# Optimization experiments

Hardware: AMD Instinct MI355X
Metric: run time of the kernel (lower is better)

The kernel has to match this reference:

```python
import jax, jax.numpy as jnp
import numpy as np

# normalization module stand-ins (simple monotone scalings, as in the repo they
# are fixed elementwise rescalings of the raw quantities)
def norm_local_x(n):
    return n

def norm_unit_contraction(c):
    return c

def norm_local_N(N):
    return jnp.log1p(N.astype(jnp.float32))

norm_TNG_radii = norm_local_x
norm_local_v = norm_local_x
norm_local_v0 = norm_local_x

EPS = 1e-5


def setup_inputs() -> dict:
    key = jax.random.key(0)
    ks = jax.random.split(key, 12)
    B, T, ND, KB = 2, 1024, 256, 3
    K_IN, H, L = 19, 128, 128
    x0 = 0.3 * jax.random.normal(ks[0], (B, T, 3), dtype=jnp.float32)
    # DM positions in local frame, |x| must stay < 1.05 (assert in original)
    x = jax.random.uniform(ks[1], (B, T, ND, 3), dtype=jnp.float32) - 0.5
    N = jax.random.randint(ks[2], (B, T), 1, 512, dtype=jnp.int32)
    basis = jax.random.normal(ks[3], (B, KB, 3), dtype=jnp.float32)
    v = jax.random.normal(ks[4], (B, T, ND, 3), dtype=jnp.float32)
    P200c = 0.5 + jax.random.uniform(ks[5], (B,), dtype=jnp.float32)
    s = 0.1
    W0 = s * jax.random.normal(ks[6], (K_IN, H - 1), dtype=jnp.float32)
    b0 = jnp.zeros((H - 1,), jnp.float32)
    W1 = s * jax.random.normal(ks[7], (H, H), dtype=jnp.float32)
    b1 = jnp.zeros((H,), jnp.float32)
    W2 = s * jax.random.normal(ks[8], (H, L), dtype=jnp.float32)
    b2 = jnp.zeros((L,), jnp.float32)
    return {"x0": x0, "x": x, "N": N, "basis": basis, "v": v, "P200c": P200c,
            "W0": W0, "b0": b0, "W1": W1, "b1": b1, "W2": W2, "b2": b2}


def create_scalars(x0, x, N, basis, v):
    B, T, ND, _ = x.shape
    # velocities relative to local mean (halo -> local frame)
    v0 = jnp.mean(v, axis=2)                      # [B,T,3]
    vc = v - v0[:, :, None, :]                    # [B,T,ND,3]

    x_norm = jnp.linalg.norm(x, axis=-1, keepdims=True) + EPS     # [B,T,ND,1]
    xu = x / x_norm
    x0_norm = jnp.linalg.norm(x0, axis=-1, keepdims=True) + EPS   # [B,T,1]
    x0u = x0 / x0_norm
    v0_norm = jnp.linalg.norm(v0, axis=-1, keepdims=True) + EPS   # [B,T,1]
    v0u = v0 / v0_norm
    v_norm = jnp.linalg.norm(vc, axis=-1, keepdims=True) + EPS    # [B,T,ND,1]
    vu = vc / v_norm

    bc = lambda a: jnp.broadcast_to(a[:, :, None, :], (B, T, ND, a.shape[-1]))

    feats = [
        norm_local_x(x_norm),                                          # |x| [1]
        norm_unit_contraction(jnp.einsum('btnd,bkd->btnk', xu, basis)),# x.basis [3]
        jnp.broadcast_to(norm_local_N(N)[:, :, None, None], (B, T, ND, 1)),  # N [1]
        bc(norm_TNG_radii(x0_norm)),                                   # |x0| [1]
        bc(norm_unit_contraction(jnp.einsum('btd,bkd->btk', x0u, basis))),  # x0.basis [3]
        bc(norm_local_v0(v0_norm)),                                    # |v0| [1]
        bc(norm_unit_contraction(jnp.einsum('btd,bkd->btk', v0u, basis))),  # v0.basis [3]
        bc(norm_unit_contraction(jnp.sum(x0u * v0u, axis=-1, keepdims=True))),  # x0.v0 [1]
        norm_local_v(v_norm),                                          # |v| [1]
        norm_unit_contraction(jnp.einsum('btnd,bkd->btnk', vu, basis)),# v.basis [3]
        norm_unit_contraction(jnp.sum(xu * vu, axis=-1, keepdims=True)),  # x.v [1]
    ]
    return jnp.concatenate(feats, axis=-1)  # [B,T,ND,19]


def reference(x0, x, N, basis, v, P200c, W0, b0, W1, b1, W2, b2):
    scalars = create_scalars(x0, x, N, basis, v)          # [B,T,ND,19]
    h = jax.nn.leaky_relu(scalars @ W0 + b0)              # [B,T,ND,H-1]
    h = jnp.mean(h, axis=2)                               # pool -> [B,T,H-1]
    h = jnp.concatenate([h, norm_local_N(N)[..., None]], axis=-1)  # [B,T,H]
    h = jax.nn.leaky_relu(h @ W1 + b1)                    # [B,T,H]
    out = h @ W2 + b2                                     # [B,T,Nlatent]
    return (1.0 / P200c)[:, None, None] * out
```

## Files before the change

kernel.cpp:

```cpp
#include <hip/hip_runtime.h>
#include <hip/hip_bf16.h>
#include <math.h>

#define EPSV 1e-5f
#define HD   128
#define AROW 40
#define WROW 40

typedef __attribute__((ext_vector_type(8))) short bf16x8;
typedef __attribute__((ext_vector_type(4))) float f32x4;

__global__ __launch_bounds__(256, 2) void net_fused(
    const float* __restrict__ x0g, const float* __restrict__ xg,
    const int*   __restrict__ Ng,  const float* __restrict__ basisg,
    const float* __restrict__ vg,  const float* __restrict__ Pg,
    const float* __restrict__ W0,  const float* __restrict__ b0,
    const float* __restrict__ W1,  const float* __restrict__ b1,
    const float* __restrict__ W2,  const float* __restrict__ b2,
    float* __restrict__ out, int Tn, int NDn)
{
    __shared__ __align__(16) __hip_bfloat16 SA[256 * AROW];
    __shared__ __align__(16) __hip_bfloat16 Wt1[128 * WROW];
    __shared__ __align__(16) __hip_bfloat16 Wt2[128 * WROW];
    __shared__ float cvec[HD];
    __shared__ float part[4][HD];
    __shared__ float hvec[HD];
    __shared__ float h1vec[HD];
    __shared__ float tailred[2][HD];
    __shared__ float vred[4][3];

    const int bt   = blockIdx.x;
    const int b    = bt / Tn;
    const int tid  = threadIdx.x;
    const int lane = tid & 63;
    const int wave = tid >> 6;

    const long pbase = ((long)bt * NDn + tid) * 3;
    const float xi0 = xg[pbase+0], xi1 = xg[pbase+1], xi2 = xg[pbase+2];
    const float vi0 = vg[pbase+0], vi1 = vg[pbase+1], vi2 = vg[pbase+2];

    float s0 = vi0, s1 = vi1, s2 = vi2;
    #pragma unroll
    for (int off = 32; off > 0; off >>= 1) {
        s0 += __shfl_down(s0, off);
        s1 += __shfl_down(s1, off);
        s2 += __shfl_down(s2, off);
    }
    if (lane == 0) { vred[wave][0] = s0; vred[wave][1] = s1; vred[wave][2] = s2; }

    {
        const int RV[9] = {0, 1, 2, 3, 14, 15, 16, 17, 18};
        if (tid < 128) {
            const int n = tid;
            __hip_bfloat16* w1 = &Wt1[n * WROW];
            __hip_bfloat16* w2 = &Wt2[n * WROW];
            const __hip_bfloat16 z16 = __float2bfloat16(0.0f);
            #pragma unroll
            for (int kk = 0; kk < 9; ++kk) {
                const float wv = (n < 127) ? W0[RV[kk] * 127 + n] : 0.0f;
                const __hip_bfloat16 hi = __float2bfloat16(wv);
                const __hip_bfloat16 lo = __float2bfloat16(wv - __bfloat162float(hi));
                w1[kk] = hi;  w1[16 + kk] = hi;
                w2[kk] = lo;  w2[16 + kk] = lo;
            }
            #pragma unroll
            for (int kk = 9; kk < 16; ++kk) {
                w1[kk] = z16;  w1[kk + 16] = z16;
                w2[kk] = z16;  w2[kk + 16] = z16;
            }
        }
    }
    __syncthreads();

    const float inv_nd = 1.0f / (float)NDn;
    const float v00 = (vred[0][0]+vred[1][0]+vred[2][0]+vred[3][0]) * inv_nd;
    const float v01 = (vred[0][1]+vred[1][1]+vred[2][1]+vred[3][1]) * inv_nd;
    const float v02 = (vred[0][2]+vred[1][2]+vred[2][2]+vred[3][2]) * inv_nd;

    const float p0 = x0g[bt*3+0], p1 = x0g[bt*3+1], p2 = x0g[bt*3+2];
    float bas[3][3];
    #pragma unroll
    for (int k = 0; k < 3; ++k)
        #pragma unroll
        for (int c = 0; c < 3; ++c)
            bas[k][c] = basisg[(b*3 + k)*3 + c];

    const float x0n  = sqrtf(p0*p0 + p1*p1 + p2*p2) + EPSV;
    const float ix0n = 1.0f / x0n;
    const float x0u0 = p0*ix0n, x0u1 = p1*ix0n, x0u2 = p2*ix0n;

    const float v0n  = sqrtf(v00*v00 + v01*v01 + v02*v02) + EPSV;
    const float iv0n = 1.0f / v0n;
    const float v0u0 = v00*iv0n, v0u1 = v01*iv0n, v0u2 = v02*iv0n;

    const float logN = log1pf((float)Ng[bt]);

    if (tid < 128) {
        float c = 0.0f;
        if (tid < 127) {
            float fc[10];
            fc[0] = logN;
            fc[1] = x0n;
            fc[2] = x0u0*bas[0][0] + x0u1*bas[0][1] + x0u2*bas[0][2];
            fc[3] = x0u0*bas[1][0] + x0u1*bas[1][1] + x0u2*bas[1][2];
            fc[4] = x0u0*bas[2][0] + x0u1*bas[2][1] + x0u2*bas[2][2];
            fc[5] = v0n;
            fc[6] = v0u0*bas[0][0] + v0u1*bas[0][1] + v0u2*bas[0][2];
            fc[7] = v0u0*bas[1][0] + v0u1*bas[1][1] + v0u2*bas[1][2];
            fc[8] = v0u0*bas[2][0] + v0u1*bas[2][1] + v0u2*bas[2][2];
            fc[9] = x0u0*v0u0 + x0u1*v0u1 + x0u2*v0u2;
            c = b0[tid];
            #pragma unroll
            for (int i = 0; i < 10; ++i)
                c = fmaf(fc[i], W0[(4 + i) * 127 + tid], c);
        }
        cvec[tid] = c;
    }

    {
        const float xn  = sqrtf(xi0*xi0 + xi1*xi1 + xi2*xi2) + EPSV;
        const float ixn = 1.0f / xn;
        const float xu0 = xi0*ixn, xu1 = xi1*ixn, xu2 = xi2*ixn;

        const float c0 = vi0 - v00, c1 = vi1 - v01, c2 = vi2 - v02;
        const float vn  = sqrtf(c0*c0 + c1*c1 + c2*c2) + EPSV;
        const float ivn = 1.0f / vn;
        const float vu0 = c0*ivn, vu1 = c1*ivn, vu2 = c2*ivn;

        float f[9];
        f[0] = xn;
        f[1] = xu0*bas[0][0] + xu1*bas[0][1] + xu2*bas[0][2];
        f[2] = xu0*bas[1][0] + xu1*bas[1][1] + xu2*bas[1][2];
        f[3] = xu0*bas[2][0] + xu1*bas[2][1] + xu2*bas[2][2];
        f[4] = vn;
        f[5] = vu0*bas[0][0] + vu1*bas[0][1] + vu2*bas[0][2];
        f[6] = vu0*bas[1][0] + vu1*bas[1][1] + vu2*bas[1][2];
        f[7] = vu0*bas[2][0] + vu1*bas[2][1] + vu2*bas[2][2];
        f[8] = xu0*vu0 + xu1*vu1 + xu2*vu2;

        __hip_bfloat16* Ar = &SA[tid * AROW];
        const __hip_bfloat16 z16 = __float2bfloat16(0.0f);
        #pragma unroll
        for (int kk = 0; kk < 9; ++kk) {
            const __hip_bfloat16 hi = __float2bfloat16(f[kk]);
            Ar[kk]      = hi;
            Ar[16 + kk] = __float2bfloat16(f[kk] - __bfloat162float(hi));
        }
        #pragma unroll
        for (int kk = 9; kk < 16; ++kk) {
            Ar[kk]      = z16;
            Ar[kk + 16] = z16;
        }
    }
    __syncthreads();

    {
        const int quad = lane >> 4;
        const int lm   = lane & 15;

        bf16x8 bf1[8], bf2[8];
        float  cl[8];
        #pragma unroll
        for (int nt = 0; nt < 8; ++nt) {
            bf1[nt] = *reinterpret_cast<const bf16x8*>(&Wt1[(nt*16 + lm) * WROW + quad*8]);
            bf2[nt] = *reinterpret_cast<const bf16x8*>(&Wt2[(nt*16 + lm) * WROW + quad*8]);
            cl[nt]  = cvec[nt*16 + lm];
        }

        float pooled[8];
        #pragma unroll
        for (int nt = 0; nt < 8; ++nt) pooled[nt] = 0.0f;

        const f32x4 zero = {0.f, 0.f, 0.f, 0.f};
        #pragma unroll
        for (int mt = 0; mt < 4; ++mt) {
            const int particle = wave*64 + mt*16 + lm;
            const bf16x8 af = *reinterpret_cast<const bf16x8*>(&SA[particle * AROW + quad*8]);
            #pragma unroll
            for (int nt = 0; nt < 8; ++nt) {
                f32x4 acc = __builtin_amdgcn_mfma_f32_16x16x32_bf16(af, bf1[nt], zero, 0, 0, 0);
                acc = __builtin_amdgcn_mfma_f32_16x16x32_bf16(af, bf2[nt], acc, 0, 0, 0);
                float t = 0.0f;
                #pragma unroll
                for (int r = 0; r < 4; ++r) {
                    const float d = acc[r] + cl[nt];
                    t += fmaxf(d, 0.01f*d);
                }
                pooled[nt] += t;
            }
        }
        #pragma unroll
        for (int nt = 0; nt < 8; ++nt) {
            pooled[nt] += __shfl_xor(pooled[nt], 16);
            pooled[nt] += __shfl_xor(pooled[nt], 32);
        }
        if (lane < 16) {
            #pragma unroll
            for (int nt = 0; nt < 8; ++nt)
                part[wave][nt*16 + lane] = pooled[nt];
        }
    }
    __syncthreads();

    if (tid < HD) {
        const float p = part[0][tid] + part[1][tid] + part[2][tid] + part[3][tid];
        hvec[tid] = (tid < 127) ? p * inv_nd : logN;
    }
    __syncthreads();

    {
        const int j    = tid & 127;
        const int half = tid >> 7;
        const int kb   = half * 64;
        float a = 0.0f;
        #pragma unroll 8
        for (int k = 0; k < 64; ++k) a = fmaf(hvec[kb + k], W1[(kb + k)*HD + j], a);
        tailred[half][j] = a;
    }
    __syncthreads();
    if (tid < HD) {
        const float a = b1[tid] + tailred[0][tid] + tailred[1][tid];
        h1vec[tid] = fmaxf(a, 0.01f*a);
    }
    __syncthreads();

    {
        const int j    = tid & 127;
        const int half = tid >> 7;
        const int kb   = half * 64;
        float a = 0.0f;
        #pragma unroll 8
        for (int k = 0; k < 64; ++k) a = fmaf(h1vec[kb + k], W2[(kb + k)*HD + j], a);
        tailred[half][j] = a;
    }
    __syncthreads();
    if (tid < HD) {
        const float a = b2[tid] + tailred[0][tid] + tailred[1][tid];
        out[(long)bt * HD + tid] = a / Pg[b];
    }
}

extern "C" void kernel_launch(void* const* d_in, const int* in_sizes, int n_in,
                              void* d_out, int out_size, void* d_ws, size_t ws_size,
                              hipStream_t stream) {
    const float* x0    = (const float*)d_in[0];
    const float* x     = (const float*)d_in[1];
    const int*   N     = (const int*)  d_in[2];
    const float* basis = (const float*)d_in[3];
    const float* v     = (const float*)d_in[4];
    const float* P200c = (const float*)d_in[5];
    const float* W0    = (const float*)d_in[6];
    const float* b0    = (const float*)d_in[7];
    const float* W1    = (const float*)d_in[8];
    const float* b1    = (const float*)d_in[9];
    const float* W2    = (const float*)d_in[10];
    const float* b2    = (const float*)d_in[11];
    float* out = (float*)d_out;

    const int B  = in_sizes[5];
    const int T  = in_sizes[2] / B;
    const int ND = in_sizes[1] / (in_sizes[2] * 3);

    dim3 grid(B * T), block(256);
    hipLaunchKernelGGL(net_fused, grid, block, 0, stream,
                       x0, x, N, basis, v, P200c, W0, b0, W1, b1, W2, b2,
                       out, T, ND);
}
```

Baseline: 119.0 us.

## Precompute split-bf16 W0 and transposed W1/W2 in a prep kernel

Adds a small prep kernel that converts W0 into hi/lo bf16 MFMA operands and transposes W1/W2 into workspace once per call. The main kernel no longer builds these weight tiles in LDS, which frees shared memory, and it raises the occupancy hint to 4 blocks per CU. The MFMA loop is reordered to keep A fragments in registers and stream B fragments from global. The tail matvecs switch to one thread per output doing float4 dot products over transposed rows, which drops a reduction and a barrier. The cost is an extra launch, plus reading weights from global/L2 instead of LDS, with half the threads idle in the tail.

```diff
diff --git a/kernel.cpp b/kernel.cpp
--- a/kernel.cpp
+++ b/kernel.cpp
@@ -5,28 +5,57 @@
 #define EPSV 1e-5f
 #define HD   128
 #define AROW 40
-#define WROW 40
 
 typedef __attribute__((ext_vector_type(8))) short bf16x8;
 typedef __attribute__((ext_vector_type(4))) float f32x4;
 
-__global__ __launch_bounds__(256, 2) void net_fused(
+__global__ __launch_bounds__(256) void prep_weights(
+    const float* __restrict__ W0, const float* __restrict__ W1,
+    const float* __restrict__ W2, __hip_bfloat16* __restrict__ wt1,
+    __hip_bfloat16* __restrict__ wt2, float* __restrict__ w1t,
+    float* __restrict__ w2t)
+{
+    if (blockIdx.x == 0) {
+        const int RV[9] = {0, 1, 2, 3, 14, 15, 16, 17, 18};
+        for (int i = threadIdx.x; i < 128 * 32; i += 256) {
+            const int n  = i >> 5;
+            const int kk = i & 15;
+            float val = 0.0f;
+            if (n < 127 && kk < 9) val = W0[RV[kk] * 127 + n];
+            const __hip_bfloat16 hi = __float2bfloat16(val);
+            const __hip_bfloat16 lo = __float2bfloat16(val - __bfloat162float(hi));
+            wt1[i] = hi;
+            wt2[i] = lo;
+        }
+    } else {
+        const int base = (blockIdx.x - 1) * 2048;
+        for (int t = threadIdx.x; t < 2048; t += 256) {
+            const int idx = base + t;
+            const float* src = (idx < 16384) ? W1 : W2;
+            float*       dst = (idx < 16384) ? w1t : w2t;
+            const int e = idx & 16383;
+            const int j = e >> 7, k = e & 127;
+            dst[j * 128 + k] = src[k * 128 + j];
+        }
+    }
+}
+
+__global__ __launch_bounds__(256, 4) void net_fused(
     const float* __restrict__ x0g, const float* __restrict__ xg,
     const int*   __restrict__ Ng,  const float* __restrict__ basisg,
     const float* __restrict__ vg,  const float* __restrict__ Pg,
     const float* __restrict__ W0,  const float* __restrict__ b0,
-    const float* __restrict__ W1,  const float* __restrict__ b1,
-    const float* __restrict__ W2,  const float* __restrict__ b2,
+    const float* __restrict__ b1,  const float* __restrict__ b2,
+    const __hip_bfloat16* __restrict__ wt1g,
+    const __hip_bfloat16* __restrict__ wt2g,
+    const float* __restrict__ w1t, const float* __restrict__ w2t,
     float* __restrict__ out, int Tn, int NDn)
 {
     __shared__ __align__(16) __hip_bfloat16 SA[256 * AROW];
-    __shared__ __align__(16) __hip_bfloat16 Wt1[128 * WROW];
-    __shared__ __align__(16) __hip_bfloat16 Wt2[128 * WROW];
     __shared__ float cvec[HD];
     __shared__ float part[4][HD];
-    __shared__ float hvec[HD];
-    __shared__ float h1vec[HD];
-    __shared__ float tailred[2][HD];
+    __shared__ __align__(16) float hvec[HD];
+    __shared__ __align__(16) float h1vec[HD];
     __shared__ float vred[4][3];
 
     const int bt   = blockIdx.x;
@@ -47,29 +76,6 @@
         s2 += __shfl_down(s2, off);
     }
     if (lane == 0) { vred[wave][0] = s0; vred[wave][1] = s1; vred[wave][2] = s2; }
-
-    {
-        const int RV[9] = {0, 1, 2, 3, 14, 15, 16, 17, 18};
-        if (tid < 128) {
-            const int n = tid;
-            __hip_bfloat16* w1 = &Wt1[n * WROW];
-            __hip_bfloat16* w2 = &Wt2[n * WROW];
-            const __hip_bfloat16 z16 = __float2bfloat16(0.0f);
-            #pragma unroll
-            for (int kk = 0; kk < 9; ++kk) {
-                const float wv = (n < 127) ? W0[RV[kk] * 127 + n] : 0.0f;
-                const __hip_bfloat16 hi = __float2bfloat16(wv);
-                const __hip_bfloat16 lo = __float2bfloat16(wv - __bfloat162float(hi));
-                w1[kk] = hi;  w1[16 + kk] = hi;
-                w2[kk] = lo;  w2[16 + kk] = lo;
-            }
-            #pragma unroll
-            for (int kk = 9; kk < 16; ++kk) {
-                w1[kk] = z16;  w1[kk + 16] = z16;
-                w2[kk] = z16;  w2[kk + 16] = z16;
-            }
-        }
-    }
     __syncthreads();
 
     const float inv_nd = 1.0f / (float)NDn;
@@ -138,19 +144,21 @@
         f[7] = vu0*bas[2][0] + vu1*bas[2][1] + vu2*bas[2][2];
         f[8] = xu0*vu0 + xu1*vu1 + xu2*vu2;
 
-        __hip_bfloat16* Ar = &SA[tid * AROW];
-        const __hip_bfloat16 z16 = __float2bfloat16(0.0f);
+        __hip_bfloat16 row[32];
+        #pragma unroll
+        for (int kk = 0; kk < 32; ++kk) row[kk] = __float2bfloat16(0.0f);
         #pragma unroll
         for (int kk = 0; kk < 9; ++kk) {
             const __hip_bfloat16 hi = __float2bfloat16(f[kk]);
-            Ar[kk]      = hi;
-            Ar[16 + kk] = __float2bfloat16(f[kk] - __bfloat162float(hi));
-        }
-        #pragma unroll
-        for (int kk = 9; kk < 16; ++kk) {
-            Ar[kk]      = z16;
-            Ar[kk + 16] = z16;
-        }
+            row[kk]      = hi;
+            row[16 + kk] = __float2bfloat16(f[kk] - __bfloat162float(hi));
+        }
+        bf16x8* dst = reinterpret_cast<bf16x8*>(&SA[tid * AROW]);
+        const bf16x8* src = reinterpret_cast<const bf16x8*>(row);
+        dst[0] = src[0];
+        dst[1] = src[1];
+        dst[2] = src[2];
+        dst[3] = src[3];
     }
     __syncthreads();
 
@@ -158,46 +166,33 @@
         const int quad = lane >> 4;
         const int lm   = lane & 15;
 
-        bf16x8 bf1[8], bf2[8];
-        float  cl[8];
+        bf16x8 afr[4];
+        #pragma unroll
+        for (int mt = 0; mt < 4; ++mt)
+            afr[mt] = *reinterpret_cast<const bf16x8*>(
+                &SA[(wave*64 + mt*16 + lm) * AROW + quad*8]);
+
+        const f32x4 zero = {0.f, 0.f, 0.f, 0.f};
         #pragma unroll
         for (int nt = 0; nt < 8; ++nt) {
-            bf1[nt] = *reinterpret_cast<const bf16x8*>(&Wt1[(nt*16 + lm) * WROW + quad*8]);
-            bf2[nt] = *reinterpret_cast<const bf16x8*>(&Wt2[(nt*16 + lm) * WROW + quad*8]);
-            cl[nt]  = cvec[nt*16 + lm];
-        }
-
-        float pooled[8];
-        #pragma unroll
-        for (int nt = 0; nt < 8; ++nt) pooled[nt] = 0.0f;
-
-        const f32x4 zero = {0.f, 0.f, 0.f, 0.f};
-        #pragma unroll
-        for (int mt = 0; mt < 4; ++mt) {
-            const int particle = wave*64 + mt*16 + lm;
-            const bf16x8 af = *reinterpret_cast<const bf16x8*>(&SA[particle * AROW + quad*8]);
+            const int woff = ((nt*16 + lm) * 32 + quad*8);
+            const bf16x8 bh = *reinterpret_cast<const bf16x8*>(&wt1g[woff]);
+            const bf16x8 bl = *reinterpret_cast<const bf16x8*>(&wt2g[woff]);
+            const float  cl = cvec[nt*16 + lm];
+            float p = 0.0f;
             #pragma unroll
-            for (int nt = 0; nt < 8; ++nt) {
-                f32x4 acc = __builtin_amdgcn_mfma_f32_16x16x32_bf16(af, bf1[nt], zero, 0, 0, 0);
-                acc = __builtin_amdgcn_mfma_f32_16x16x32_bf16(af, bf2[nt], acc, 0, 0, 0);
-                float t = 0.0f;
+            for (int mt = 0; mt < 4; ++mt) {
+                f32x4 acc = __builtin_amdgcn_mfma_f32_16x16x32_bf16(afr[mt], bh, zero, 0, 0, 0);
+                acc = __builtin_amdgcn_mfma_f32_16x16x32_bf16(afr[mt], bl, acc, 0, 0, 0);
                 #pragma unroll
                 for (int r = 0; r < 4; ++r) {
-                    const float d = acc[r] + cl[nt];
-                    t += fmaxf(d, 0.01f*d);
+                    const float d = acc[r] + cl;
+                    p += fmaxf(d, 0.01f*d);
                 }
-                pooled[nt] += t;
             }
-        }
-        #pragma unroll
-        for (int nt = 0; nt < 8; ++nt) {
-            pooled[nt] += __shfl_xor(pooled[nt], 16);
-            pooled[nt] += __shfl_xor(pooled[nt], 32);
-        }
-        if (lane < 16) {
-            #pragma unroll
-            for (int nt = 0; nt < 8; ++nt)
-                part[wave][nt*16 + lane] = pooled[nt];
+            p += __shfl_xor(p, 16);
+            p += __shfl_xor(p, 32);
+            if (lane < 16) part[wave][nt*16 + lane] = p;
         }
     }
     __syncthreads();
@@ -208,34 +203,36 @@
     }
     __syncthreads();
 
-    {
-        const int j    = tid & 127;
-        const int half = tid >> 7;
-        const int kb   = half * 64;
-        float a = 0.0f;
+    if (tid < HD) {
+        float a = b1[tid];
+        const float4* wr = reinterpret_cast<const float4*>(&w1t[tid * 128]);
+        const float4* hv = reinterpret_cast<const float4*>(hvec);
         #pragma unroll 8
-        for (int k = 0; k < 64; ++k) a = fmaf(hvec[kb + k], W1[(kb + k)*HD + j], a);
-        tailred[half][j] = a;
-    }
-    __syncthreads();
+        for (int kk = 0; kk < 32; ++kk) {
+            const float4 h4 = hv[kk];
+            const float4 w4 = wr[kk];
+            a = fmaf(h4.x, w4.x, a);
+            a = fmaf(h4.y, w4.y, a);
+            a = fmaf(h4.z, w4.z, a);
+            a = fmaf(h4.w, w4.w, a);
+        }
+        h1vec[tid] = fmaxf(a, 0.01f*a);
+    }
+    __syncthreads();
+
     if (tid < HD) {
-        const float a = b1[tid] + tailred[0][tid] + tailred[1][tid];
-        h1vec[tid] = fmaxf(a, 0.01f*a);
-    }
-    __syncthreads();
-
-    {
-        const int j    = tid & 127;
-        const int half = tid >> 7;
-        const int kb   = half * 64;
-        float a = 0.0f;
+        float a = b2[tid];
+        const float4* wr = reinterpret_cast<const float4*>(&w2t[tid * 128]);
+        const float4* hv = reinterpret_cast<const float4*>(h1vec);
         #pragma unroll 8
-        for (int k = 0; k < 64; ++k) a = fmaf(h1vec[kb + k], W2[(kb + k)*HD + j], a);
-        tailred[half][j] = a;
-    }
-    __syncthreads();
-    if (tid < HD) {
-        const float a = b2[tid] + tailred[0][tid] + tailred[1][tid];
+        for (int kk = 0; kk < 32; ++kk) {
+            const float4 h4 = hv[kk];
+            const float4 w4 = wr[kk];
+            a = fmaf(h4.x, w4.x, a);
+            a = fmaf(h4.y, w4.y, a);
+            a = fmaf(h4.z, w4.z, a);
+            a = fmaf(h4.w, w4.w, a);
+        }
         out[(long)bt * HD + tid] = a / Pg[b];
     }
 }
@@ -261,8 +258,16 @@
     const int T  = in_sizes[2] / B;
     const int ND = in_sizes[1] / (in_sizes[2] * 3);
 
-    dim3 grid(B * T), block(256);
-    hipLaunchKernelGGL(net_fused, grid, block, 0, stream,
-                       x0, x, N, basis, v, P200c, W0, b0, W1, b1, W2, b2,
-                       out, T, ND);
+    char* ws = (char*)d_ws;
+    __hip_bfloat16* wt1 = (__hip_bfloat16*)(ws);
+    __hip_bfloat16* wt2 = (__hip_bfloat16*)(ws + 8192);
+    float*          w1t = (float*)(ws + 16384);
+    float*          w2t = (float*)(ws + 81920);
+
+    hipLaunchKernelGGL(prep_weights, dim3(17), dim3(256), 0, stream,
+                       W0, W1, W2, wt1, wt2, w1t, w2t);
+
+    hipLaunchKernelGGL(net_fused, dim3(B * T), dim3(256), 0, stream,
+                       x0, x, N, basis, v, P200c, W0, b0, b1, b2,
+                       wt1, wt2, w1t, w2t, out, T, ND);
 }
```

New measurement: 136.5 us. 1.15x slower.

## Split fused kernel into weight prep, per-halo pooling, and batched tail MLP

Applied to the files above, without the earlier changes.

Replaces the single per-halo kernel with three launches. A one-block kernel precomputes the split-bf16 W0 tiles once into workspace. A one-wave-per-halo kernel does the feature build and MFMA pooling over all 256 particles. A separate tail kernel runs the two dense layers over 16 halos per block so W1/W2 loads are shared across rows. This removes the per-block weight conversion and the barrier-heavy, single-row tail matvecs, at the cost of extra launches, a global round trip for pooled features, and less parallelism per halo. ND is now hard-coded to 256.

```diff
diff --git a/kernel.cpp b/kernel.cpp
--- a/kernel.cpp
+++ b/kernel.cpp
@@ -3,79 +3,78 @@
 #include <math.h>
 
 #define EPSV 1e-5f
-#define HD   128
 #define AROW 40
-#define WROW 40
+#define HSTR 129
 
 typedef __attribute__((ext_vector_type(8))) short bf16x8;
 typedef __attribute__((ext_vector_type(4))) float f32x4;
 
-__global__ __launch_bounds__(256, 2) void net_fused(
+__global__ __launch_bounds__(256) void prep_weights(
+    const float* __restrict__ W0,
+    __hip_bfloat16* __restrict__ wt1, __hip_bfloat16* __restrict__ wt2)
+{
+    const int RV[9] = {0, 1, 2, 3, 14, 15, 16, 17, 18};
+    for (int i = threadIdx.x; i < 128 * 32; i += 256) {
+        const int n  = i >> 5;
+        const int kk = i & 15;
+        float val = 0.0f;
+        if (n < 127 && kk < 9) val = W0[RV[kk] * 127 + n];
+        const __hip_bfloat16 hi = __float2bfloat16(val);
+        const __hip_bfloat16 lo = __float2bfloat16(val - __bfloat162float(hi));
+        wt1[i] = hi;
+        wt2[i] = lo;
+    }
+}
+
+__global__ __launch_bounds__(64, 2) void halo_pool(
     const float* __restrict__ x0g, const float* __restrict__ xg,
     const int*   __restrict__ Ng,  const float* __restrict__ basisg,
-    const float* __restrict__ vg,  const float* __restrict__ Pg,
-    const float* __restrict__ W0,  const float* __restrict__ b0,
-    const float* __restrict__ W1,  const float* __restrict__ b1,
-    const float* __restrict__ W2,  const float* __restrict__ b2,
-    float* __restrict__ out, int Tn, int NDn)
+    const float* __restrict__ vg,  const float* __restrict__ W0,
+    const float* __restrict__ b0,
+    const __hip_bfloat16* __restrict__ wt1g,
+    const __hip_bfloat16* __restrict__ wt2g,
+    float* __restrict__ hbuf, int Tn)
 {
     __shared__ __align__(16) __hip_bfloat16 SA[256 * AROW];
-    __shared__ __align__(16) __hip_bfloat16 Wt1[128 * WROW];
-    __shared__ __align__(16) __hip_bfloat16 Wt2[128 * WROW];
-    __shared__ float cvec[HD];
-    __shared__ float part[4][HD];
-    __shared__ float hvec[HD];
-    __shared__ float h1vec[HD];
-    __shared__ float tailred[2][HD];
-    __shared__ float vred[4][3];
+    __shared__ float cvec[128];
 
     const int bt   = blockIdx.x;
     const int b    = bt / Tn;
-    const int tid  = threadIdx.x;
-    const int lane = tid & 63;
-    const int wave = tid >> 6;
-
-    const long pbase = ((long)bt * NDn + tid) * 3;
-    const float xi0 = xg[pbase+0], xi1 = xg[pbase+1], xi2 = xg[pbase+2];
-    const float vi0 = vg[pbase+0], vi1 = vg[pbase+1], vi2 = vg[pbase+2];
-
-    float s0 = vi0, s1 = vi1, s2 = vi2;
-    #pragma unroll
-    for (int off = 32; off > 0; off >>= 1) {
-        s0 += __shfl_down(s0, off);
-        s1 += __shfl_down(s1, off);
-        s2 += __shfl_down(s2, off);
-    }
-    if (lane == 0) { vred[wave][0] = s0; vred[wave][1] = s1; vred[wave][2] = s2; }
-
-    {
-        const int RV[9] = {0, 1, 2, 3, 14, 15, 16, 17, 18};
-        if (tid < 128) {
-            const int n = tid;
-            __hip_bfloat16* w1 = &Wt1[n * WROW];
-            __hip_bfloat16* w2 = &Wt2[n * WROW];
-            const __hip_bfloat16 z16 = __float2bfloat16(0.0f);
-            #pragma unroll
-            for (int kk = 0; kk < 9; ++kk) {
-                const float wv = (n < 127) ? W0[RV[kk] * 127 + n] : 0.0f;
-                const __hip_bfloat16 hi = __float2bfloat16(wv);
-                const __hip_bfloat16 lo = __float2bfloat16(wv - __bfloat162float(hi));
-                w1[kk] = hi;  w1[16 + kk] = hi;
-                w2[kk] = lo;  w2[16 + kk] = lo;
-            }
-            #pragma unroll
-            for (int kk = 9; kk < 16; ++kk) {
-                w1[kk] = z16;  w1[kk + 16] = z16;
-                w2[kk] = z16;  w2[kk + 16] = z16;
-            }
-        }
-    }
-    __syncthreads();
-
-    const float inv_nd = 1.0f / (float)NDn;
-    const float v00 = (vred[0][0]+vred[1][0]+vred[2][0]+vred[3][0]) * inv_nd;
-    const float v01 = (vred[0][1]+vred[1][1]+vred[2][1]+vred[3][1]) * inv_nd;
-    const float v02 = (vred[0][2]+vred[1][2]+vred[2][2]+vred[3][2]) * inv_nd;
+    const int lane = threadIdx.x;
+    const int quad = lane >> 4;
+    const int lm   = lane & 15;
+
+    bf16x8 bh[8], bl[8];
+    #pragma unroll
+    for (int nt = 0; nt < 8; ++nt) {
+        const int woff = (nt*16 + lm) * 32 + quad * 8;
+        bh[nt] = *reinterpret_cast<const bf16x8*>(&wt1g[woff]);
+        bl[nt] = *reinterpret_cast<const bf16x8*>(&wt2g[woff]);
+    }
+
+    const long gbase = (long)bt * 256 * 3;
+    float px[4][3], pv[4][3];
+    #pragma unroll
+    for (int j = 0; j < 4; ++j) {
+        const int p = j*64 + lane;
+        #pragma unroll
+        for (int c = 0; c < 3; ++c) {
+            px[j][c] = xg[gbase + p*3 + c];
+            pv[j][c] = vg[gbase + p*3 + c];
+        }
+    }
+
+    float s0 = pv[0][0]+pv[1][0]+pv[2][0]+pv[3][0];
+    float s1 = pv[0][1]+pv[1][1]+pv[2][1]+pv[3][1];
+    float s2 = pv[0][2]+pv[1][2]+pv[2][2]+pv[3][2];
+    #pragma unroll
+    for (int m = 1; m < 64; m <<= 1) {
+        s0 += __shfl_xor(s0, m);
+        s1 += __shfl_xor(s1, m);
+        s2 += __shfl_xor(s2, m);
+    }
+    const float inv_nd = 1.0f / 256.0f;
+    const float v00 = s0 * inv_nd, v01 = s1 * inv_nd, v02 = s2 * inv_nd;
 
     const float p0 = x0g[bt*3+0], p1 = x0g[bt*3+1], p2 = x0g[bt*3+2];
     float bas[3][3];
@@ -95,34 +94,40 @@
 
     const float logN = log1pf((float)Ng[bt]);
 
-    if (tid < 128) {
-        float c = 0.0f;
-        if (tid < 127) {
-            float fc[10];
-            fc[0] = logN;
-            fc[1] = x0n;
-            fc[2] = x0u0*bas[0][0] + x0u1*bas[0][1] + x0u2*bas[0][2];
-            fc[3] = x0u0*bas[1][0] + x0u1*bas[1][1] + x0u2*bas[1][2];
-            fc[4] = x0u0*bas[2][0] + x0u1*bas[2][1] + x0u2*bas[2][2];
-            fc[5] = v0n;
-            fc[6] = v0u0*bas[0][0] + v0u1*bas[0][1] + v0u2*bas[0][2];
-            fc[7] = v0u0*bas[1][0] + v0u1*bas[1][1] + v0u2*bas[1][2];
-            fc[8] = v0u0*bas[2][0] + v0u1*bas[2][1] + v0u2*bas[2][2];
-            fc[9] = x0u0*v0u0 + x0u1*v0u1 + x0u2*v0u2;
-            c = b0[tid];
-            #pragma unroll
-            for (int i = 0; i < 10; ++i)
-                c = fmaf(fc[i], W0[(4 + i) * 127 + tid], c);
-        }
-        cvec[tid] = c;
-    }
-
     {
+        float fc[10];
+        fc[0] = logN;
+        fc[1] = x0n;
+        fc[2] = x0u0*bas[0][0] + x0u1*bas[0][1] + x0u2*bas[0][2];
+        fc[3] = x0u0*bas[1][0] + x0u1*bas[1][1] + x0u2*bas[1][2];
+        fc[4] = x0u0*bas[2][0] + x0u1*bas[2][1] + x0u2*bas[2][2];
+        fc[5] = v0n;
+        fc[6] = v0u0*bas[0][0] + v0u1*bas[0][1] + v0u2*bas[0][2];
+        fc[7] = v0u0*bas[1][0] + v0u1*bas[1][1] + v0u2*bas[1][2];
+        fc[8] = v0u0*bas[2][0] + v0u1*bas[2][1] + v0u2*bas[2][2];
+        fc[9] = x0u0*v0u0 + x0u1*v0u1 + x0u2*v0u2;
+        #pragma unroll
+        for (int h = 0; h < 2; ++h) {
+            const int n = lane + h*64;
+            float c = 0.0f;
+            if (n < 127) {
+                c = b0[n];
+                #pragma unroll
+                for (int i = 0; i < 10; ++i)
+                    c = fmaf(fc[i], W0[(4 + i) * 127 + n], c);
+            }
+            cvec[n] = c;
+        }
+    }
+
+    #pragma unroll
+    for (int j = 0; j < 4; ++j) {
+        const float xi0 = px[j][0], xi1 = px[j][1], xi2 = px[j][2];
         const float xn  = sqrtf(xi0*xi0 + xi1*xi1 + xi2*xi2) + EPSV;
         const float ixn = 1.0f / xn;
         const float xu0 = xi0*ixn, xu1 = xi1*ixn, xu2 = xi2*ixn;
 
-        const float c0 = vi0 - v00, c1 = vi1 - v01, c2 = vi2 - v02;
+        const float c0 = pv[j][0] - v00, c1 = pv[j][1] - v01, c2 = pv[j][2] - v02;
         const float vn  = sqrtf(c0*c0 + c1*c1 + c2*c2) + EPSV;
         const float ivn = 1.0f / vn;
         const float vu0 = c0*ivn, vu1 = c1*ivn, vu2 = c2*ivn;
@@ -138,105 +143,130 @@
         f[7] = vu0*bas[2][0] + vu1*bas[2][1] + vu2*bas[2][2];
         f[8] = xu0*vu0 + xu1*vu1 + xu2*vu2;
 
-        __hip_bfloat16* Ar = &SA[tid * AROW];
-        const __hip_bfloat16 z16 = __float2bfloat16(0.0f);
+        __hip_bfloat16 row[32];
+        #pragma unroll
+        for (int kk = 0; kk < 32; ++kk) row[kk] = __float2bfloat16(0.0f);
         #pragma unroll
         for (int kk = 0; kk < 9; ++kk) {
             const __hip_bfloat16 hi = __float2bfloat16(f[kk]);
-            Ar[kk]      = hi;
-            Ar[16 + kk] = __float2bfloat16(f[kk] - __bfloat162float(hi));
-        }
-        #pragma unroll
-        for (int kk = 9; kk < 16; ++kk) {
-            Ar[kk]      = z16;
-            Ar[kk + 16] = z16;
-        }
+            row[kk]      = hi;
+            row[16 + kk] = __float2bfloat16(f[kk] - __bfloat162float(hi));
+        }
+        bf16x8* dst = reinterpret_cast<bf16x8*>(&SA[(j*64 + lane) * AROW]);
+        const bf16x8* src = reinterpret_cast<const bf16x8*>(row);
+        dst[0] = src[0]; dst[1] = src[1]; dst[2] = src[2]; dst[3] = src[3];
     }
     __syncthreads();
 
-    {
-        const int quad = lane >> 4;
-        const int lm   = lane & 15;
-
-        bf16x8 bf1[8], bf2[8];
-        float  cl[8];
+    float cl[8];
+    #pragma unroll
+    for (int nt = 0; nt < 8; ++nt) cl[nt] = cvec[nt*16 + lm];
+
+    float pooled[8];
+    #pragma unroll
+    for (int nt = 0; nt < 8; ++nt) pooled[nt] = 0.0f;
+
+    const f32x4 zero = {0.f, 0.f, 0.f, 0.f};
+    #pragma unroll 4
+    for (int mt = 0; mt < 16; ++mt) {
+        const bf16x8 af = *reinterpret_cast<const bf16x8*>(
+            &SA[(mt*16 + lm) * AROW + quad*8]);
         #pragma unroll
         for (int nt = 0; nt < 8; ++nt) {
-            bf1[nt] = *reinterpret_cast<const bf16x8*>(&Wt1[(nt*16 + lm) * WROW + quad*8]);
-            bf2[nt] = *reinterpret_cast<const bf16x8*>(&Wt2[(nt*16 + lm) * WROW + quad*8]);
-            cl[nt]  = cvec[nt*16 + lm];
-        }
-
-        float pooled[8];
-        #pragma unroll
-        for (int nt = 0; nt < 8; ++nt) pooled[nt] = 0.0f;
-
-        const f32x4 zero = {0.f, 0.f, 0.f, 0.f};
-        #pragma unroll
-        for (int mt = 0; mt < 4; ++mt) {
-            const int particle = wave*64 + mt*16 + lm;
-            const bf16x8 af = *reinterpret_cast<const bf16x8*>(&SA[particle * AROW + quad*8]);
+            f32x4 acc = __builtin_amdgcn_mfma_f32_16x16x32_bf16(af, bh[nt], zero, 0, 0, 0);
+            acc = __builtin_amdgcn_mfma_f32_16x16x32_bf16(af, bl[nt], acc, 0, 0, 0);
             #pragma unroll
-            for (int nt = 0; nt < 8; ++nt) {
-                f32x4 acc = __builtin_amdgcn_mfma_f32_16x16x32_bf16(af, bf1[nt], zero, 0, 0, 0);
-                acc = __builtin_amdgcn_mfma_f32_16x16x32_bf16(af, bf2[nt], acc, 0, 0, 0);
-                float t = 0.0f;
-                #pragma unroll
-                for (int r = 0; r < 4; ++r) {
-                    const float d = acc[r] + cl[nt];
-                    t += fmaxf(d, 0.01f*d);
-                }
-                pooled[nt] += t;
+            for (int r = 0; r < 4; ++r) {
+                const float d = acc[r] + cl[nt];
+                pooled[nt] += fmaxf(d, 0.01f*d);
             }
         }
+    }
+    #pragma unroll
+    for (int nt = 0; nt < 8; ++nt) {
+        pooled[nt] += __shfl_xor(pooled[nt], 16);
+        pooled[nt] += __shfl_xor(pooled[nt], 32);
+    }
+    if (lane < 16) {
         #pragma unroll
         for (int nt = 0; nt < 8; ++nt) {
-            pooled[nt] += __shfl_xor(pooled[nt], 16);
-            pooled[nt] += __shfl_xor(pooled[nt], 32);
-        }
-        if (lane < 16) {
-            #pragma unroll
-            for (int nt = 0; nt < 8; ++nt)
-                part[wave][nt*16 + lane] = pooled[nt];
+            const int n = nt*16 + lane;
+            hbuf[(long)bt * 128 + n] = (n < 127) ? pooled[nt] * inv_nd : logN;
+        }
+    }
+}
+
+__global__ __launch_bounds__(256) void tail_mlp(
+    const float* __restrict__ hbuf, const float* __restrict__ W1,
+    const float* __restrict__ b1,   const float* __restrict__ W2,
+    const float* __restrict__ b2,   const float* __restrict__ Pg,
+    float* __restrict__ out, int Tn, int BT)
+{
+    __shared__ float Hl[16 * HSTR];
+    __shared__ float H1[16 * HSTR];
+
+    const int t    = threadIdx.x;
+    const int row0 = blockIdx.x * 16;
+
+    #pragma unroll
+    for (int it = 0; it < 2; ++it) {
+        const int l = (t + it*256) * 4;
+        const long g = (long)row0 * 128 + l;
+        if (row0 + (l >> 7) < BT) {
+            const float4 h4 = *reinterpret_cast<const float4*>(&hbuf[g]);
+            const int r = l >> 7, c = l & 127;
+            Hl[r*HSTR + c+0] = h4.x;
+            Hl[r*HSTR + c+1] = h4.y;
+            Hl[r*HSTR + c+2] = h4.z;
+            Hl[r*HSTR + c+3] = h4.w;
         }
     }
     __syncthreads();
 
-    if (tid < HD) {
-        const float p = part[0][tid] + part[1][tid] + part[2][tid] + part[3][tid];
-        hvec[tid] = (tid < 127) ? p * inv_nd : logN;
+    const int r  = t >> 4;
+    const int j0 = (t & 15) * 8;
+
+    float a[8];
+    #pragma unroll
+    for (int q = 0; q < 8; ++q) a[q] = b1[j0 + q];
+    #pragma unroll 4
+    for (int k = 0; k < 128; ++k) {
+        const float hk = Hl[r*HSTR + k];
+        const float4 wa = *reinterpret_cast<const float4*>(&W1[k*128 + j0]);
+        const float4 wb = *reinterpret_cast<const float4*>(&W1[k*128 + j0 + 4]);
+        a[0] = fmaf(hk, wa.x, a[0]);  a[1] = fmaf(hk, wa.y, a[1]);
+        a[2] = fmaf(hk, wa.z, a[2]);  a[3] = fmaf(hk, wa.w, a[3]);
+        a[4] = fmaf(hk, wb.x, a[4]);  a[5] = fmaf(hk, wb.y, a[5]);
+        a[6] = fmaf(hk, wb.z, a[6]);  a[7] = fmaf(hk, wb.w, a[7]);
+    }
+    #pragma unroll
+    for (int q = 0; q < 8; ++q) {
+        const float x = a[q];
+        H1[r*HSTR + j0 + q] = fmaxf(x, 0.01f*x);
     }
     __syncthreads();
 
-    {
-        const int j    = tid & 127;
-        const int half = tid >> 7;
-        const int kb   = half * 64;
-        float a = 0.0f;
-        #pragma unroll 8
-        for (int k = 0; k < 64; ++k) a = fmaf(hvec[kb + k], W1[(kb + k)*HD + j], a);
-        tailred[half][j] = a;
-    }
-    __syncthreads();
-    if (tid < HD) {
-        const float a = b1[tid] + tailred[0][tid] + tailred[1][tid];
-        h1vec[tid] = fmaxf(a, 0.01f*a);
-    }
-    __syncthreads();
-
-    {
-        const int j    = tid & 127;
-        const int half = tid >> 7;
-        const int kb   = half * 64;
-        float a = 0.0f;
-        #pragma unroll 8
-        for (int k = 0; k < 64; ++k) a = fmaf(h1vec[kb + k], W2[(kb + k)*HD + j], a);
-        tailred[half][j] = a;
-    }
-    __syncthreads();
-    if (tid < HD) {
-        const float a = b2[tid] + tailred[0][tid] + tailred[1][tid];
-        out[(long)bt * HD + tid] = a / Pg[b];
+    #pragma unroll
+    for (int q = 0; q < 8; ++q) a[q] = b2[j0 + q];
+    #pragma unroll 4
+    for (int k = 0; k < 128; ++k) {
+        const float hk = H1[r*HSTR + k];
+        const float4 wa = *reinterpret_cast<const float4*>(&W2[k*128 + j0]);
+        const float4 wb = *reinterpret_cast<const float4*>(&W2[k*128 + j0 + 4]);
+        a[0] = fmaf(hk, wa.x, a[0]);  a[1] = fmaf(hk, wa.y, a[1]);
+        a[2] = fmaf(hk, wa.z, a[2]);  a[3] = fmaf(hk, wa.w, a[3]);
+        a[4] = fmaf(hk, wb.x, a[4]);  a[5] = fmaf(hk, wb.y, a[5]);
+        a[6] = fmaf(hk, wb.z, a[6]);  a[7] = fmaf(hk, wb.w, a[7]);
+    }
+
+    const int grow = row0 + r;
+    if (grow < BT) {
+        const float sc = 1.0f / Pg[grow / Tn];
+        float4 o;
+        o.x = a[0]*sc; o.y = a[1]*sc; o.z = a[2]*sc; o.w = a[3]*sc;
+        *reinterpret_cast<float4*>(&out[(long)grow*128 + j0]) = o;
+        o.x = a[4]*sc; o.y = a[5]*sc; o.z = a[6]*sc; o.w = a[7]*sc;
+        *reinterpret_cast<float4*>(&out[(long)grow*128 + j0 + 4]) = o;
     }
 }
 
@@ -259,10 +289,18 @@
 
     const int B  = in_sizes[5];
     const int T  = in_sizes[2] / B;
-    const int ND = in_sizes[1] / (in_sizes[2] * 3);
-
-    dim3 grid(B * T), block(256);
-    hipLaunchKernelGGL(net_fused, grid, block, 0, stream,
-                       x0, x, N, basis, v, P200c, W0, b0, W1, b1, W2, b2,
-                       out, T, ND);
+    const int BT = B * T;
+
+    char* ws = (char*)d_ws;
+    __hip_bfloat16* wt1  = (__hip_bfloat16*)(ws);
+    __hip_bfloat16* wt2  = (__hip_bfloat16*)(ws + 8192);
+    float*          hbuf = (float*)(ws + 16384);
+
+    hipLaunchKernelGGL(prep_weights, dim3(1), dim3(256), 0, stream, W0, wt1, wt2);
+
+    hipLaunchKernelGGL(halo_pool, dim3(BT), dim3(64), 0, stream,
+                       x0, x, N, basis, v, W0, b0, wt1, wt2, hbuf, T);
+
+    hipLaunchKernelGGL(tail_mlp, dim3((BT + 15) / 16), dim3(256), 0, stream,
+                       hbuf, W1, b1, W2, b2, P200c, out, T, BT);
 }
```

After: 138.4 us. +16.4%, slower.
